# Performance work log

Measured on AMD Instinct MI355X. Metric: run time of the kernel, lower is better.

The kernel has to match this reference:

```python
import jax, jax.numpy as jnp
import numpy as np
import math

L, B, D, H = 2048, 4, 1024, 16
DK = D // H
DFF = 4 * D
EPS = 1e-5


def setup_inputs() -> dict:
    key = jax.random.key(0)
    ks = jax.random.split(key, 16)
    s = 1.0 / math.sqrt(D)
    sf = 1.0 / math.sqrt(DFF)
    return {
        "x": jax.random.normal(ks[0], (L, B, D), jnp.float32),
        "Wq": jax.random.normal(ks[1], (D, D), jnp.float32) * s,
        "bq": jnp.zeros((D,), jnp.float32),
        "Wk": jax.random.normal(ks[2], (D, D), jnp.float32) * s,
        "bk": jnp.zeros((D,), jnp.float32),
        "Wv": jax.random.normal(ks[3], (D, D), jnp.float32) * s,
        "bv": jnp.zeros((D,), jnp.float32),
        "Wo": jax.random.normal(ks[4], (D, D), jnp.float32) * s,
        "bo": jnp.zeros((D,), jnp.float32),
        "W1": jax.random.normal(ks[5], (D, DFF), jnp.float32) * s,
        "b1": jnp.zeros((DFF,), jnp.float32),
        "W2": jax.random.normal(ks[6], (DFF, D), jnp.float32) * sf,
        "b2": jnp.zeros((D,), jnp.float32),
        "g1": jnp.ones((D,), jnp.float32),
        "be1": jnp.zeros((D,), jnp.float32),
        "g2": jnp.ones((D,), jnp.float32),
        "be2": jnp.zeros((D,), jnp.float32),
    }


def _layer_norm(x, g, b):
    mu = jnp.mean(x, axis=-1, keepdims=True)
    var = jnp.var(x, axis=-1, keepdims=True)
    return (x - mu) * jax.lax.rsqrt(var + EPS) * g + b


def reference(x, Wq, bq, Wk, bk, Wv, bv, Wo, bo, W1, b1, W2, b2, g1, be1, g2, be2):
    # x: (L, B, D)
    q = x @ Wq + bq
    k = x @ Wk + bk
    v = x @ Wv + bv
    # (L,B,H,dk) -> (B,H,L,dk)
    q = q.reshape(L, B, H, DK).transpose(1, 2, 0, 3)
    k = k.reshape(L, B, H, DK).transpose(1, 2, 0, 3)
    v = v.reshape(L, B, H, DK).transpose(1, 2, 0, 3)
    scale = 1.0 / math.sqrt(DK)
    scores = jnp.einsum('bhqd,bhkd->bhqk', q, k) * scale
    w = jax.nn.softmax(scores, axis=-1)
    attn = jnp.einsum('bhqk,bhkd->bhqd', w, v)  # (B,H,L,dk)
    attn = attn.transpose(2, 0, 1, 3).reshape(L, B, D)
    attn_out = attn @ Wo + bo
    x = _layer_norm(x + attn_out, g1, be1)
    h = jax.nn.gelu(x @ W1 + b1, approximate=False)
    ff = h @ W2 + b2
    return _layer_norm(x + ff, g2, be2)
```

## Files before the change

### kernel.cpp

```cpp
#include <hip/hip_runtime.h>

#define L_   2048
#define B_   4
#define D_   1024
#define H_   16
#define DK_  64
#define DFF_ 4096
#define NT_  (L_*B_)

typedef unsigned short u16;
typedef unsigned int   u32;
typedef __bf16 bf16x8 __attribute__((ext_vector_type(8)));
typedef float  f32x4  __attribute__((ext_vector_type(4)));

__device__ __forceinline__ u16 f2bf(float f) {
  u32 u = __float_as_uint(f);
  u += 0x7fffu + ((u >> 16) & 1u);
  return (u16)(u >> 16);
}
__device__ __forceinline__ float bf2f(u32 lo16) {
  return __uint_as_float(lo16 << 16);
}

#define GLDS16(g, l) __builtin_amdgcn_global_load_lds( \
    (const __attribute__((address_space(1))) void*)(g), \
    (__attribute__((address_space(3))) void*)(l), 16, 0, 0)

#define SCQ_ 0.18033688011112042f

__global__ __launch_bounds__(256) void transpose_w_k(
    const float* __restrict__ W, u16* __restrict__ Wt, int K, int N)
{
  __shared__ float tile[32][33];
  int n0 = blockIdx.x * 32, k0 = blockIdx.y * 32;
  int tx = threadIdx.x, ty = threadIdx.y;
#pragma unroll
  for (int i = ty; i < 32; i += 8)
    tile[i][tx] = W[(size_t)(k0 + i) * N + n0 + tx];
  __syncthreads();
#pragma unroll
  for (int i = ty; i < 32; i += 8)
    Wt[(size_t)(n0 + i) * K + k0 + tx] = f2bf(tile[tx][i]);
}

__global__ __launch_bounds__(256) void transpose_w4_k(
    const float* __restrict__ W0, const float* __restrict__ W1,
    const float* __restrict__ W2, const float* __restrict__ W3,
    u16* __restrict__ dst)
{
  __shared__ float tile[32][33];
  int z = blockIdx.z;
  const float* W = (z == 0) ? W0 : (z == 1) ? W1 : (z == 2) ? W2 : W3;
  u16* Wt = dst + (size_t)z * 1048576;
  int n0 = blockIdx.x * 32, k0 = blockIdx.y * 32;
  int tx = threadIdx.x, ty = threadIdx.y;
#pragma unroll
  for (int i = ty; i < 32; i += 8)
    tile[i][tx] = W[(size_t)(k0 + i) * 1024 + n0 + tx];
  __syncthreads();
#pragma unroll
  for (int i = ty; i < 32; i += 8)
    Wt[(size_t)(n0 + i) * 1024 + k0 + tx] = f2bf(tile[tx][i]);
}

__global__ __launch_bounds__(256) void f32_to_bf16_k(
    const float* __restrict__ in, u16* __restrict__ out, int n4)
{
  int i = blockIdx.x * 256 + threadIdx.x;
  if (i >= n4) return;
  float4 v = ((const float4*)in)[i];
  uint2 r;
  r.x = (u32)f2bf(v.x) | ((u32)f2bf(v.y) << 16);
  r.y = (u32)f2bf(v.z) | ((u32)f2bf(v.w) << 16);
  ((uint2*)out)[i] = r;
}

__global__ __launch_bounds__(256) void bias_concat_k(
    const float* __restrict__ bq, const float* __restrict__ bk,
    const float* __restrict__ bv, float* __restrict__ o)
{
  int i = blockIdx.x * 256 + threadIdx.x;
  float v = (i < 1024) ? bq[i] : ((i < 2048) ? bk[i - 1024] : bv[i - 2048]);
  o[i] = v;
}

template<int BN, int EPI>
__global__ __launch_bounds__(512, 2)
void gemm_pipe(const u16* __restrict__ A, const u16* __restrict__ Bt,
               const float* __restrict__ bias, const void* __restrict__ res,
               u16* __restrict__ outb, int M, int N, int K)
{
  constexpr int BM = 256;
  constexpr int NI  = 2 + BN / 128;
  constexpr int NWN = BN / 64;
  constexpr int NWM = 8 / NWN;
  constexpr int MIT = (BM / NWM) / 16;
  constexpr int NPH = MIT / 4;
  constexpr int BUFB = (BM + BN) * 64;
  __shared__ char SM[4 * BUFB];

  const int tid = threadIdx.x;
  const int w = tid >> 6, lane = tid & 63;
  const int l15 = lane & 15, l4 = lane >> 4;
  const int NK = K >> 5;

  const int gx = gridDim.x;
  int nwg = gx * gridDim.y;
  int id = blockIdx.y * gx + blockIdx.x;
  int q = nwg >> 3, r = nwg & 7;
  int xcd = id & 7, idx = id >> 3;
  int wg = (xcd < r ? xcd * (q + 1) : r * (q + 1) + (xcd - r) * q) + idx;
  const int m0 = (wg / gx) * BM, n0 = (wg % gx) * BN;
  const int wm = (w / NWN) * (BM / NWM), wn = (w % NWN) * 64;

  const u16* gsrc[NI];
#pragma unroll
  for (int k = 0; k < NI; ++k) {
    int o = k * 8192 + tid * 16;
    int col8 = (((o >> 4) ^ (o >> 6)) & 3);
    if (o < BM * 64) {
      int rrow = o >> 6;
      gsrc[k] = A + (size_t)(m0 + rrow) * K + col8 * 8;
    } else {
      int br = (o - BM * 64) >> 6;
      gsrc[k] = Bt + (size_t)(n0 + br) * K + col8 * 8;
    }
  }

  auto stage = [&](int t3, int k) {
    const u16* s = (t3 < NK) ? gsrc[k] + (size_t)t3 * 32 : gsrc[k];
    GLDS16(s, SM + (t3 & 3) * BUFB + k * 8192 + w * 1024);
  };

  for (int t3 = 0; t3 < 3; ++t3)
#pragma unroll
    for (int k = 0; k < NI; ++k) stage(t3, k);
  if constexpr (BN == 256) asm volatile("s_waitcnt vmcnt(8)" ::: "memory");
  else                     asm volatile("s_waitcnt vmcnt(6)" ::: "memory");
  asm volatile("s_barrier" ::: "memory");

  f32x4 acc[MIT][4];
#pragma unroll
  for (int i = 0; i < MIT; ++i)
#pragma unroll
    for (int j = 0; j < 4; ++j) acc[i][j] = (f32x4){0.f, 0.f, 0.f, 0.f};

  const int csw = (l4 ^ (l15 & 3)) * 16;

  for (int t = 0; t < NK; ++t) {
    const char* rb = SM + (t & 3) * BUFB;
    bf16x8 bfr[4];
#pragma unroll
    for (int ph = 0; ph < NPH; ++ph) {
      bf16x8 af[4];
#pragma unroll
      for (int mi = 0; mi < 4; ++mi)
        af[mi] = *(const bf16x8*)(rb + (wm + ph * 64 + mi * 16 + l15) * 64 + csw);
      if (ph == 0) {
#pragma unroll
        for (int nj = 0; nj < 4; ++nj)
          bfr[nj] = *(const bf16x8*)(rb + BM * 64 + (wn + nj * 16 + l15) * 64 + csw);
      }
      if constexpr (NPH == 2) {
        stage(t + 3, ph * 2 + 0);
        stage(t + 3, ph * 2 + 1);
      } else {
        stage(t + 3, 0); stage(t + 3, 1); stage(t + 3, 2);
      }
      asm volatile("s_barrier" ::: "memory");
      __builtin_amdgcn_s_setprio(1);
#pragma unroll
      for (int mi = 0; mi < 4; ++mi)
#pragma unroll
        for (int nj = 0; nj < 4; ++nj)
          acc[ph * 4 + mi][nj] = __builtin_amdgcn_mfma_f32_16x16x32_bf16(
              af[mi], bfr[nj], acc[ph * 4 + mi][nj], 0, 0, 0);
      __builtin_amdgcn_s_setprio(0);
      if (ph == NPH - 1) {
        if constexpr (BN == 256) asm volatile("s_waitcnt vmcnt(8)" ::: "memory");
        else                     asm volatile("s_waitcnt vmcnt(6)" ::: "memory");
      }
      asm volatile("s_barrier" ::: "memory");
    }
  }
  asm volatile("s_waitcnt vmcnt(0)" ::: "memory");

  const int gm = m0 + wm + l4 * 4;
  const int gn = n0 + wn + l15;
#pragma unroll
  for (int mi = 0; mi < MIT; ++mi) {
#pragma unroll
    for (int nj = 0; nj < 4; ++nj) {
      int col = gn + nj * 16;
      float bv = bias[col];
#pragma unroll
      for (int rr = 0; rr < 4; ++rr) {
        int row = gm + mi * 16 + rr;
        float v = acc[mi][nj][rr] + bv;
        if (EPI == 2) {
          float gv = 0.5f * v * (1.f + erff(v * 0.70710678118654752f));
          outb[(size_t)row * N + col] = f2bf(gv);
        } else if (EPI == 3) {
          int which = col >> 10, c1 = col & 1023;
          int ll = row >> 2, bb = row & 3;
          int hh = c1 >> 6, dd = c1 & 63;
          if (which == 0) v *= SCQ_;
          outb[(size_t)which * 8388608 +
               ((((size_t)(bb * H_ + hh)) * L_ + ll) << 6) + dd] = f2bf(v);
        } else if (EPI == 5) {
          size_t idxo = (size_t)row * N + col;
          outb[idxo] = f2bf(v + ((const float*)res)[idxo]);
        } else {
          size_t idxo = (size_t)row * N + col;
          outb[idxo] = f2bf(v + bf2f(((const u16*)res)[idxo]));
        }
      }
    }
  }
}

__global__ __launch_bounds__(256, 3)
void attn_fwd2(const u16* __restrict__ qp, const u16* __restrict__ kp,
               const u16* __restrict__ vp, u16* __restrict__ op)
{
  __shared__ u16 Ks[2][64 * 64];
  __shared__ u16 Vt[2][64 * 64];
  const int tid = threadIdx.x, w = tid >> 6, lane = tid & 63;
  const int l15 = lane & 15, l4 = lane >> 4;
  const int n = blockIdx.x;
  const int bh = (n & 7) | ((n >> 7) << 3);
  const int qi = (n >> 3) & 15;
  const int q0 = qi * 128;
  const u16* qb = qp + (size_t)bh * L_ * DK_;
  const u16* kb = kp + (size_t)bh * L_ * DK_;
  const u16* vb = vp + (size_t)bh * L_ * DK_;

  bf16x8 qf[2][2];
#pragma unroll
  for (int g = 0; g < 2; ++g)
#pragma unroll
    for (int kk = 0; kk < 2; ++kk)
      qf[g][kk] = *(const bf16x8*)&qb[(size_t)(q0 + g * 64 + w * 16 + l15) * DK_ +
                                      kk * 32 + l4 * 8];

  f32x4 accO[2][4];
  f32x4 lacc[2];
#pragma unroll
  for (int g = 0; g < 2; ++g) {
#pragma unroll
    for (int i = 0; i < 4; ++i) accO[g][i] = (f32x4){0.f, 0.f, 0.f, 0.f};
    lacc[g] = (f32x4){0.f, 0.f, 0.f, 0.f};
  }

  bf16x8 oneb;
  {
    u32 ob = (l15 == 0) ? 0x3f803f80u : 0u;
#pragma unroll
    for (int j = 0; j < 4; ++j) ((u32*)&oneb)[j] = ob;
  }

  int rho0 = tid >> 3, rho1 = (256 + tid) >> 3, cseg = lane & 7;
  int kv0 = (rho0 & 32) | ((rho0 & 12) << 1) | ((rho0 & 16) >> 2) | (rho0 & 3);
  int kv1 = (rho1 & 32) | ((rho1 & 12) << 1) | ((rho1 & 16) >> 2) | (rho1 & 3);
  const u16* ksrc0 = kb + (size_t)kv0 * DK_ + ((cseg ^ (rho0 & 7)) << 3);
  const u16* ksrc1 = kb + (size_t)kv1 * DK_ + ((cseg ^ (rho1 & 7)) << 3);

  const int vseg = tid & 7, vkvp = tid >> 3;
  const u16* vsrc = vb + (size_t)(vkvp * 2) * DK_ + vseg * 8;
  u32 voff[8];
#pragma unroll
  for (int dd2 = 0; dd2 < 4; ++dd2) {
    int d0 = vseg * 8 + dd2 * 2, d1 = d0 + 1;
    voff[dd2 * 2] = d0 * 128 +
        ((((vkvp >> 2) ^ (d0 & 7) ^ (d0 >> 3)) << 4) | ((vkvp & 3) << 2));
    voff[dd2 * 2 + 1] = d1 * 128 +
        ((((vkvp >> 2) ^ (d1 & 7) ^ (d1 >> 3)) << 4) | ((vkvp & 3) << 2));
  }

  auto packV = [&](int buf, uint4 a, uint4 b) {
#pragma unroll
    for (int dd2 = 0; dd2 < 4; ++dd2) {
      u32 ai = ((const u32*)&a)[dd2], bi = ((const u32*)&b)[dd2];
      *(u32*)((char*)Vt[buf] + voff[dd2 * 2])     = __builtin_amdgcn_perm(bi, ai, 0x05040100u);
      *(u32*)((char*)Vt[buf] + voff[dd2 * 2 + 1]) = __builtin_amdgcn_perm(bi, ai, 0x07060302u);
    }
  };

  auto exp_pack = [&](f32x4 (&s)[4], u32 (&pk)[2][4]) {
#pragma unroll
    for (int i = 0; i < 4; ++i)
#pragma unroll
      for (int rr = 0; rr < 4; ++rr) s[i][rr] = exp2f(s[i][rr]);
#pragma unroll
    for (int kk = 0; kk < 2; ++kk)
#pragma unroll
      for (int j2 = 0; j2 < 4; ++j2) {
        int nb = kk * 2 + (j2 >> 1);
        int rr = (j2 & 1) * 2;
        u32 rres;
        asm("v_cvt_pk_bf16_f32 %0, %1, %2" : "=v"(rres)
            : "v"(s[nb][rr]), "v"(s[nb][rr + 1]));
        pk[kk][j2] = rres;
      }
  };

  {
    uint4 a = *(const uint4*)vsrc;
    uint4 b = *(const uint4*)(vsrc + DK_);
    GLDS16(ksrc0, &Ks[0][w * 512]);
    GLDS16(ksrc1, &Ks[0][2048 + w * 512]);
    packV(0, a, b);
  }
  __syncthreads();

  constexpr int NTI = L_ / 64;
  for (int t = 0; t < NTI; ++t) {
    const int cur = t & 1;
    const bool pf = (t + 1 < NTI);
    const int tn = pf ? t + 1 : t;

    uint4 va = *(const uint4*)(vsrc + (size_t)(tn * 64) * DK_);
    uint4 vbv = *(const uint4*)(vsrc + (size_t)(tn * 64) * DK_ + DK_);
    if (pf) {
      GLDS16(ksrc0 + (size_t)((t + 1) * 64) * DK_, &Ks[cur ^ 1][w * 512]);
      GLDS16(ksrc1 + (size_t)((t + 1) * 64) * DK_, &Ks[cur ^ 1][2048 + w * 512]);
    }

    f32x4 s0[4], s1[4];
#pragma unroll
    for (int i = 0; i < 4; ++i) {
      s0[i] = (f32x4){0.f, 0.f, 0.f, 0.f};
      s1[i] = (f32x4){0.f, 0.f, 0.f, 0.f};
    }
#pragma unroll
    for (int kk = 0; kk < 2; ++kk) {
#pragma unroll
      for (int nb = 0; nb < 4; ++nb) {
        int row = nb * 16 + l15;
        bf16x8 kf = *(const bf16x8*)((const char*)Ks[cur] + row * 128 +
                                     (((kk * 4 + l4) ^ (row & 7)) << 4));
        s0[nb] = __builtin_amdgcn_mfma_f32_16x16x32_bf16(kf, qf[0][kk], s0[nb], 0, 0, 0);
        s1[nb] = __builtin_amdgcn_mfma_f32_16x16x32_bf16(kf, qf[1][kk], s1[nb], 0, 0, 0);
      }
    }

    u32 pk0[2][4], pk1[2][4];
    exp_pack(s0, pk0);
    exp_pack(s1, pk1);

    if (pf) packV(cur ^ 1, va, vbv);

#pragma unroll
    for (int kk = 0; kk < 2; ++kk) {
      bf16x8 pa0, pa1;
      ((u32*)&pa0)[0] = pk0[kk][0]; ((u32*)&pa0)[1] = pk0[kk][1];
      ((u32*)&pa0)[2] = pk0[kk][2]; ((u32*)&pa0)[3] = pk0[kk][3];
      ((u32*)&pa1)[0] = pk1[kk][0]; ((u32*)&pa1)[1] = pk1[kk][1];
      ((u32*)&pa1)[2] = pk1[kk][2]; ((u32*)&pa1)[3] = pk1[kk][3];
      lacc[0] = __builtin_amdgcn_mfma_f32_16x16x32_bf16(pa0, oneb, lacc[0], 0, 0, 0);
      lacc[1] = __builtin_amdgcn_mfma_f32_16x16x32_bf16(pa1, oneb, lacc[1], 0, 0, 0);
#pragma unroll
      for (int nb2 = 0; nb2 < 4; ++nb2) {
        int drow = nb2 * 16 + l15;
        bf16x8 vf = *(const bf16x8*)((const char*)Vt[cur] + drow * 128 +
                                     (((kk * 4 + l4) ^ (drow & 7) ^ (drow >> 3)) << 4));
        accO[0][nb2] = __builtin_amdgcn_mfma_f32_16x16x32_bf16(pa0, vf, accO[0][nb2], 0, 0, 0);
        accO[1][nb2] = __builtin_amdgcn_mfma_f32_16x16x32_bf16(pa1, vf, accO[1][nb2], 0, 0, 0);
      }
    }
    __syncthreads();
  }

  const int bb = bh >> 4, hh = bh & 15;
#pragma unroll
  for (int g = 0; g < 2; ++g) {
#pragma unroll
    for (int rr = 0; rr < 4; ++rr) {
      float ls = __shfl(lacc[g][rr], l4 << 4);
      float rl = 1.f / ls;
      int qg = q0 + g * 64 + w * 16 + l4 * 4 + rr;
      size_t base = ((size_t)qg * B_ + bb) * D_ + hh * 64;
#pragma unroll
      for (int nb2 = 0; nb2 < 4; ++nb2)
        op[base + nb2 * 16 + l15] = f2bf(accO[g][nb2][rr] * rl);
    }
  }
}

__global__ __launch_bounds__(256) void layernorm_bf_k(
    const u16* __restrict__ y, const float* __restrict__ g, const float* __restrict__ be,
    float* __restrict__ of, u16* __restrict__ ob)
{
  int row = blockIdx.x, tid = threadIdx.x;
  uint2 raw = *(const uint2*)&y[(size_t)row * D_ + tid * 4];
  float v0 = bf2f(raw.x & 0xffffu), v1 = bf2f(raw.x >> 16);
  float v2 = bf2f(raw.y & 0xffffu), v3 = bf2f(raw.y >> 16);
  float s = (v0 + v1) + (v2 + v3);
  float ss = v0 * v0 + v1 * v1 + v2 * v2 + v3 * v3;
#pragma unroll
  for (int msk = 32; msk >= 1; msk >>= 1) {
    s += __shfl_xor(s, msk);
    ss += __shfl_xor(ss, msk);
  }
  __shared__ float rs[4], rss[4];
  if ((tid & 63) == 0) { rs[tid >> 6] = s; rss[tid >> 6] = ss; }
  __syncthreads();
  s = rs[0] + rs[1] + rs[2] + rs[3];
  ss = rss[0] + rss[1] + rss[2] + rss[3];
  float mu = s * (1.f / D_);
  float var = ss * (1.f / D_) - mu * mu;
  float rstd = rsqrtf(var + 1e-5f);
  int c = tid * 4;
  float o0 = (v0 - mu) * rstd * g[c + 0] + be[c + 0];
  float o1 = (v1 - mu) * rstd * g[c + 1] + be[c + 1];
  float o2 = (v2 - mu) * rstd * g[c + 2] + be[c + 2];
  float o3 = (v3 - mu) * rstd * g[c + 3] + be[c + 3];
  if (of) {
    float4 o = {o0, o1, o2, o3};
    *(float4*)&of[(size_t)row * D_ + c] = o;
  }
  if (ob) {
    uint2 r;
    r.x = (u32)f2bf(o0) | ((u32)f2bf(o1) << 16);
    r.y = (u32)f2bf(o2) | ((u32)f2bf(o3) << 16);
    *(uint2*)&ob[(size_t)row * D_ + c] = r;
  }
}

extern "C" void kernel_launch(void* const* d_in, const int* in_sizes, int n_in,
                              void* d_out, int out_size, void* d_ws, size_t ws_size,
                              hipStream_t stream)
{
  const float* x   = (const float*)d_in[0];
  const float* Wq  = (const float*)d_in[1];
  const float* bq  = (const float*)d_in[2];
  const float* Wk  = (const float*)d_in[3];
  const float* bk  = (const float*)d_in[4];
  const float* Wv  = (const float*)d_in[5];
  const float* bv  = (const float*)d_in[6];
  const float* Wo  = (const float*)d_in[7];
  const float* bo  = (const float*)d_in[8];
  const float* W1f = (const float*)d_in[9];
  const float* b1  = (const float*)d_in[10];
  const float* W2f = (const float*)d_in[11];
  const float* b2  = (const float*)d_in[12];
  const float* g1  = (const float*)d_in[13];
  const float* be1 = (const float*)d_in[14];
  const float* g2  = (const float*)d_in[15];
  const float* be2 = (const float*)d_in[16];

  char* ws = (char*)d_ws;
  const size_t MB = 1024 * 1024;
  u16* WqT  = (u16*)(ws + 0 * MB);
  u16* WoT  = (u16*)(ws + 6 * MB);
  u16* W1T  = (u16*)(ws + 8 * MB);
  u16* W2T  = (u16*)(ws + 16 * MB);
  u16* xb   = (u16*)(ws + 24 * MB);
  u16* qp   = (u16*)(ws + 40 * MB);
  u16* astd = (u16*)(ws + 88 * MB);
  u16* yb   = (u16*)(ws + 104 * MB);
  u16* x1b  = (u16*)(ws + 120 * MB);
  u16* hbuf = (u16*)(ws + 136 * MB);
  float* bcat = (float*)(ws + 200 * MB);
  u16* kp = qp + 8388608;
  u16* vp = qp + 16777216;

  dim3 tb(32, 8);
  transpose_w4_k<<<dim3(32, 32, 4), tb, 0, stream>>>(Wq, Wk, Wv, Wo, WqT);
  transpose_w_k<<<dim3(128, 32), tb, 0, stream>>>(W1f, W1T, D_, DFF_);
  transpose_w_k<<<dim3(32, 128), tb, 0, stream>>>(W2f, W2T, DFF_, D_);
  f32_to_bf16_k<<<NT_ * D_ / 4 / 256, 256, 0, stream>>>(x, xb, NT_ * D_ / 4);
  bias_concat_k<<<12, 256, 0, stream>>>(bq, bk, bv, bcat);

  gemm_pipe<128, 3><<<dim3(24, 32), 512, 0, stream>>>(
      xb, WqT, bcat, nullptr, qp, NT_, 3072, D_);

  attn_fwd2<<<1024, 256, 0, stream>>>(qp, kp, vp, astd);

  gemm_pipe<128, 5><<<dim3(8, 32), 512, 0, stream>>>(
      astd, WoT, bo, x, yb, NT_, D_, D_);
  layernorm_bf_k<<<NT_, 256, 0, stream>>>(yb, g1, be1, nullptr, x1b);
  gemm_pipe<256, 2><<<dim3(16, 32), 512, 0, stream>>>(
      x1b, W1T, b1, nullptr, hbuf, NT_, DFF_, D_);
  gemm_pipe<128, 6><<<dim3(8, 32), 512, 0, stream>>>(
      hbuf, W2T, b2, x1b, yb, NT_, D_, DFF_);
  layernorm_bf_k<<<NT_, 256, 0, stream>>>(yb, g2, be2, (float*)d_out, nullptr);
}
```

Before: 465.6 us.

## Restructure GEMM to BK=64 with triple buffering and fixed 256x128 tiles

The pipelined bf16 GEMM now uses a K-tile of 64 instead of 32, with a 3-stage LDS ring instead of 4 stages and a new 8-way XOR swizzle for 128-byte rows. Each wave computes a 64x64 sub-tile split into two K phases, and the 256-wide N tile variant is removed, so the FFN1 GEMM now launches twice as many 256x128 blocks. The aim is fewer barriers and loop iterations per unit of K and better LDS bank behaviour. In exchange, the FFN1 GEMM gets less operand reuse per block and there is one fewer prefetch stage to hide latency.

```diff
diff --git a/kernel.cpp b/kernel.cpp
--- a/kernel.cpp
+++ b/kernel.cpp
@@ -84,25 +84,21 @@
   o[i] = v;
 }
 
-template<int BN, int EPI>
+template<int EPI>
 __global__ __launch_bounds__(512, 2)
 void gemm_pipe(const u16* __restrict__ A, const u16* __restrict__ Bt,
                const float* __restrict__ bias, const void* __restrict__ res,
                u16* __restrict__ outb, int M, int N, int K)
 {
-  constexpr int BM = 256;
-  constexpr int NI  = 2 + BN / 128;
-  constexpr int NWN = BN / 64;
-  constexpr int NWM = 8 / NWN;
-  constexpr int MIT = (BM / NWM) / 16;
-  constexpr int NPH = MIT / 4;
-  constexpr int BUFB = (BM + BN) * 64;
-  __shared__ char SM[4 * BUFB];
+  constexpr int BM = 256, BN = 128, BK = 64;
+  constexpr int ABYTES = BM * BK * 2;
+  constexpr int BUFB = (BM + BN) * BK * 2;
+  __shared__ char SM[3 * BUFB];
 
   const int tid = threadIdx.x;
   const int w = tid >> 6, lane = tid & 63;
   const int l15 = lane & 15, l4 = lane >> 4;
-  const int NK = K >> 5;
+  const int NK = K >> 6;
 
   const int gx = gridDim.x;
   int nwg = gx * gridDim.y;
@@ -111,75 +107,74 @@
   int xcd = id & 7, idx = id >> 3;
   int wg = (xcd < r ? xcd * (q + 1) : r * (q + 1) + (xcd - r) * q) + idx;
   const int m0 = (wg / gx) * BM, n0 = (wg % gx) * BN;
-  const int wm = (w / NWN) * (BM / NWM), wn = (w % NWN) * 64;
-
-  const u16* gsrc[NI];
-#pragma unroll
-  for (int k = 0; k < NI; ++k) {
-    int o = k * 8192 + tid * 16;
-    int col8 = (((o >> 4) ^ (o >> 6)) & 3);
-    if (o < BM * 64) {
-      int rrow = o >> 6;
-      gsrc[k] = A + (size_t)(m0 + rrow) * K + col8 * 8;
+  const int wm = (w >> 1) * 64, wn = (w & 1) * 64;
+
+  const u16* gsrc[6];
+#pragma unroll
+  for (int u = 0; u < 6; ++u) {
+    int o = u * 8192 + tid * 16;
+    int row; const u16* base;
+    if (o < ABYTES) {
+      row = o >> 7;
+      base = A + (size_t)(m0 + row) * K;
     } else {
-      int br = (o - BM * 64) >> 6;
-      gsrc[k] = Bt + (size_t)(n0 + br) * K + col8 * 8;
-    }
-  }
-
-  auto stage = [&](int t3, int k) {
-    const u16* s = (t3 < NK) ? gsrc[k] + (size_t)t3 * 32 : gsrc[k];
-    GLDS16(s, SM + (t3 & 3) * BUFB + k * 8192 + w * 1024);
+      int ob = o - ABYTES;
+      row = ob >> 7;
+      base = Bt + (size_t)(n0 + row) * K;
+    }
+    int col8 = ((o >> 4) & 7) ^ (row & 7);
+    gsrc[u] = base + col8 * 8;
+  }
+
+  auto stage = [&](int t, int u) {
+    const u16* s = gsrc[u] + (size_t)((t < NK) ? t : 0) * BK;
+    GLDS16(s, SM + (t % 3) * BUFB + u * 8192 + w * 1024);
   };
 
-  for (int t3 = 0; t3 < 3; ++t3)
-#pragma unroll
-    for (int k = 0; k < NI; ++k) stage(t3, k);
-  if constexpr (BN == 256) asm volatile("s_waitcnt vmcnt(8)" ::: "memory");
-  else                     asm volatile("s_waitcnt vmcnt(6)" ::: "memory");
+  for (int tt = 0; tt < 2; ++tt)
+#pragma unroll
+    for (int u = 0; u < 6; ++u) stage(tt, u);
+  asm volatile("s_waitcnt vmcnt(6)" ::: "memory");
   asm volatile("s_barrier" ::: "memory");
 
-  f32x4 acc[MIT][4];
-#pragma unroll
-  for (int i = 0; i < MIT; ++i)
+  f32x4 acc[4][4];
+#pragma unroll
+  for (int i = 0; i < 4; ++i)
 #pragma unroll
     for (int j = 0; j < 4; ++j) acc[i][j] = (f32x4){0.f, 0.f, 0.f, 0.f};
 
-  const int csw = (l4 ^ (l15 & 3)) * 16;
-
   for (int t = 0; t < NK; ++t) {
-    const char* rb = SM + (t & 3) * BUFB;
-    bf16x8 bfr[4];
-#pragma unroll
-    for (int ph = 0; ph < NPH; ++ph) {
-      bf16x8 af[4];
+    const char* rb = SM + (t % 3) * BUFB;
+    const int tn = t + 2;
+#pragma unroll
+    for (int ph = 0; ph < 2; ++ph) {
+      bf16x8 af[4], bfr[4];
+#pragma unroll
+      for (int mi = 0; mi < 4; ++mi) {
+        int row = wm + mi * 16 + l15;
+        af[mi] = *(const bf16x8*)(rb + row * 128 +
+                                  (((ph * 4 + l4) ^ (l15 & 7)) << 4));
+      }
+#pragma unroll
+      for (int nj = 0; nj < 4; ++nj) {
+        int row = wn + nj * 16 + l15;
+        bfr[nj] = *(const bf16x8*)(rb + ABYTES + row * 128 +
+                                   (((ph * 4 + l4) ^ (l15 & 7)) << 4));
+      }
+      asm volatile("s_barrier" ::: "memory");
+      stage(tn, ph * 3 + 0);
+      stage(tn, ph * 3 + 1);
+      stage(tn, ph * 3 + 2);
+      __builtin_amdgcn_s_setprio(1);
 #pragma unroll
       for (int mi = 0; mi < 4; ++mi)
-        af[mi] = *(const bf16x8*)(rb + (wm + ph * 64 + mi * 16 + l15) * 64 + csw);
-      if (ph == 0) {
 #pragma unroll
         for (int nj = 0; nj < 4; ++nj)
-          bfr[nj] = *(const bf16x8*)(rb + BM * 64 + (wn + nj * 16 + l15) * 64 + csw);
-      }
-      if constexpr (NPH == 2) {
-        stage(t + 3, ph * 2 + 0);
-        stage(t + 3, ph * 2 + 1);
-      } else {
-        stage(t + 3, 0); stage(t + 3, 1); stage(t + 3, 2);
-      }
-      asm volatile("s_barrier" ::: "memory");
-      __builtin_amdgcn_s_setprio(1);
-#pragma unroll
-      for (int mi = 0; mi < 4; ++mi)
-#pragma unroll
-        for (int nj = 0; nj < 4; ++nj)
-          acc[ph * 4 + mi][nj] = __builtin_amdgcn_mfma_f32_16x16x32_bf16(
-              af[mi], bfr[nj], acc[ph * 4 + mi][nj], 0, 0, 0);
+          acc[mi][nj] = __builtin_amdgcn_mfma_f32_16x16x32_bf16(
+              af[mi], bfr[nj], acc[mi][nj], 0, 0, 0);
       __builtin_amdgcn_s_setprio(0);
-      if (ph == NPH - 1) {
-        if constexpr (BN == 256) asm volatile("s_waitcnt vmcnt(8)" ::: "memory");
-        else                     asm volatile("s_waitcnt vmcnt(6)" ::: "memory");
-      }
+      if (ph == 1)
+        asm volatile("s_waitcnt vmcnt(6)" ::: "memory");
       asm volatile("s_barrier" ::: "memory");
     }
   }
@@ -188,7 +183,7 @@
   const int gm = m0 + wm + l4 * 4;
   const int gn = n0 + wn + l15;
 #pragma unroll
-  for (int mi = 0; mi < MIT; ++mi) {
+  for (int mi = 0; mi < 4; ++mi) {
 #pragma unroll
     for (int nj = 0; nj < 4; ++nj) {
       int col = gn + nj * 16;
@@ -472,17 +467,17 @@
   f32_to_bf16_k<<<NT_ * D_ / 4 / 256, 256, 0, stream>>>(x, xb, NT_ * D_ / 4);
   bias_concat_k<<<12, 256, 0, stream>>>(bq, bk, bv, bcat);
 
-  gemm_pipe<128, 3><<<dim3(24, 32), 512, 0, stream>>>(
+  gemm_pipe<3><<<dim3(24, 32), 512, 0, stream>>>(
       xb, WqT, bcat, nullptr, qp, NT_, 3072, D_);
 
   attn_fwd2<<<1024, 256, 0, stream>>>(qp, kp, vp, astd);
 
-  gemm_pipe<128, 5><<<dim3(8, 32), 512, 0, stream>>>(
+  gemm_pipe<5><<<dim3(8, 32), 512, 0, stream>>>(
       astd, WoT, bo, x, yb, NT_, D_, D_);
   layernorm_bf_k<<<NT_, 256, 0, stream>>>(yb, g1, be1, nullptr, x1b);
-  gemm_pipe<256, 2><<<dim3(16, 32), 512, 0, stream>>>(
+  gemm_pipe<2><<<dim3(32, 32), 512, 0, stream>>>(
       x1b, W1T, b1, nullptr, hbuf, NT_, DFF_, D_);
-  gemm_pipe<128, 6><<<dim3(8, 32), 512, 0, stream>>>(
+  gemm_pipe<6><<<dim3(8, 32), 512, 0, stream>>>(
       hbuf, W2T, b2, x1b, yb, NT_, D_, DFF_);
   layernorm_bf_k<<<NT_, 256, 0, stream>>>(yb, g2, be2, (float*)d_out, nullptr);
 }
```

Result: no change. 459.5 us (-1.3%).
